# Kernel optimization log

Measured on AMD Instinct MI355X. Metric: run time of the kernel, lower is better.

## Reference

```python
import jax, jax.numpy as jnp
import numpy as np

N_EMBD = 512
HEAD_SIZE = 64
END_TOKEN = 32000  # == vocab_size


def setup_inputs() -> dict:
    key = jax.random.key(0)
    k1, k2, k3, k4, k5 = jax.random.split(key, 5)
    B, T = 16, 2048
    x = jax.random.normal(k1, (B, T, N_EMBD), dtype=jnp.float32)
    idx = jax.random.randint(k2, (B, T), 0, END_TOKEN)  # never hits END_TOKEN
    s = 1.0 / np.sqrt(N_EMBD)
    Wk = jax.random.normal(k3, (N_EMBD, HEAD_SIZE), dtype=jnp.float32) * s
    Wq = jax.random.normal(k4, (N_EMBD, HEAD_SIZE), dtype=jnp.float32) * s
    Wv = jax.random.normal(k5, (N_EMBD, HEAD_SIZE), dtype=jnp.float32) * s
    return {"x": x, "Wk": Wk, "Wq": Wq, "Wv": Wv, "idx": idx}


def reference(x, Wk, Wq, Wv, idx):
    B, T, C = x.shape
    k = x @ Wk  # [B,T,H]
    q = x @ Wq
    v = x @ Wv
    # end-token mask: zero out query rows at positions >= first end-token position
    is_end = idx == END_TOKEN                       # [B,T]
    has_end = jnp.any(is_end, axis=1)               # [B]
    first_end = jnp.argmax(is_end, axis=1)          # [B], 0 if none
    pos = jnp.arange(T)
    row_ok = jnp.where(has_end[:, None], pos[None, :] < first_end[:, None], True)  # [B,T]
    causal = jnp.tril(jnp.ones((T, T), dtype=bool))
    mask = causal[None, :, :] & row_ok[:, :, None]  # [B,T,T]
    # NOTE: original scales by C**-0.5 with C = n_embd, not head_size
    wei = jnp.einsum('bqh,bkh->bqk', q, k) * (C ** -0.5)
    wei = jnp.where(mask, wei, -jnp.inf)
    wei = jax.nn.softmax(wei, axis=-1)
    out = jnp.einsum('bqk,bkh->bqh', wei, v)  # [B,T,H]
    return out
```

## Files before the change

kernel.cpp:

```cpp
#include <hip/hip_runtime.h>
#include <hip/hip_bf16.h>


#define B_ 16
#define T_ 2048
#define C_ 512
#define LOG2E 1.4426950408889634f

typedef __attribute__((ext_vector_type(4))) float f32x4;
typedef __attribute__((ext_vector_type(8))) short bf16x8;

__device__ inline unsigned short f2bf(float f) {
    unsigned int u = __builtin_bit_cast(unsigned int, f);
    u += 0x7fff + ((u >> 16) & 1);
    return (unsigned short)(u >> 16);
}

__device__ inline f32x4 mfma16(bf16x8 a, bf16x8 b, f32x4 c) {
    return __builtin_amdgcn_mfma_f32_16x16x32_bf16(a, b, c, 0, 0, 0);
}

__global__ void prep_kernel(const float* __restrict__ Wk, const float* __restrict__ Wq,
                            const float* __restrict__ Wv, unsigned short* __restrict__ Wt,
                            int* __restrict__ fe) {
    if (blockIdx.x == 384) {
        if (threadIdx.x < B_) fe[threadIdx.x] = T_;
        return;
    }
    int id = blockIdx.x * 256 + threadIdx.x;
    int n = id >> 9, k = id & 511;
    int mtx = n >> 6, nl = n & 63;
    const float* W = (mtx == 0) ? Wk : ((mtx == 1) ? Wq : Wv);
    float v = W[k * 64 + nl];
    if (mtx == 1) v *= 0.04419417382415922f;
    Wt[n * 512 + k] = f2bf(v);
}

__global__ void scan_kernel(const int* __restrict__ idx, int* __restrict__ fe) {
    int i = blockIdx.x * 256 + threadIdx.x;
    if (idx[i] == 32000) atomicMin(&fe[i >> 11], i & 2047);
}

__global__ __launch_bounds__(256) void qkv_kernel(
        const float* __restrict__ x, const unsigned short* __restrict__ Wt,
        unsigned short* __restrict__ Qm, unsigned short* __restrict__ Km,
        unsigned short* __restrict__ Vt) {
    __shared__ __align__(16) char smem[32768];
    unsigned short* xs  = (unsigned short*)smem;
    unsigned short* wsh = (unsigned short*)(smem + 8192);
    unsigned short* co  = (unsigned short*)smem;
    unsigned short* vco = (unsigned short*)(smem + 17408);

    int tid = threadIdx.x, wave = tid >> 6, lane = tid & 63;
    int m16 = lane & 15, quad = lane >> 4;
    int row0 = blockIdx.x * 64;

    int xrow[2], xcol[2], wrow[6], wcol[6];
#pragma unroll
    for (int i = 0; i < 2; i++) { int u = tid + i * 256; xrow[i] = u >> 3; xcol[i] = (u & 7) * 8; }
#pragma unroll
    for (int i = 0; i < 6; i++) { int u = tid + i * 256; wrow[i] = u >> 3; wcol[i] = (u & 7) * 8; }

    f32x4 xa[2][2]; bf16x8 wr[6];
#pragma unroll
    for (int i = 0; i < 2; i++) {
        const f32x4* p = (const f32x4*)(x + (long)(row0 + xrow[i]) * C_ + xcol[i]);
        xa[i][0] = p[0]; xa[i][1] = p[1];
    }
#pragma unroll
    for (int i = 0; i < 6; i++) wr[i] = *(const bf16x8*)&Wt[wrow[i] * C_ + wcol[i]];

    f32x4 ka[4], qa[4], va[4];
#pragma unroll
    for (int i = 0; i < 4; i++) {
        ka[i] = (f32x4){0.f, 0.f, 0.f, 0.f};
        qa[i] = (f32x4){0.f, 0.f, 0.f, 0.f};
        va[i] = (f32x4){0.f, 0.f, 0.f, 0.f};
    }

    for (int kb = 0; kb < C_; kb += 64) {
        __syncthreads();
#pragma unroll
        for (int i = 0; i < 2; i++) {
            bf16x8 t;
#pragma unroll
            for (int j = 0; j < 4; j++) t[j] = (short)f2bf(xa[i][0][j]);
#pragma unroll
            for (int j = 0; j < 4; j++) t[4 + j] = (short)f2bf(xa[i][1][j]);
            *(bf16x8*)&xs[xrow[i] * 64 + (xcol[i] ^ ((xrow[i] & 7) * 8))] = t;
        }
#pragma unroll
        for (int i = 0; i < 6; i++)
            *(bf16x8*)&wsh[wrow[i] * 64 + (wcol[i] ^ ((wrow[i] & 7) * 8))] = wr[i];
        int kn = kb + 64;
        if (kn < C_) {
#pragma unroll
            for (int i = 0; i < 2; i++) {
                const f32x4* p = (const f32x4*)(x + (long)(row0 + xrow[i]) * C_ + kn + xcol[i]);
                xa[i][0] = p[0]; xa[i][1] = p[1];
            }
#pragma unroll
            for (int i = 0; i < 6; i++) wr[i] = *(const bf16x8*)&Wt[wrow[i] * C_ + kn + wcol[i]];
        }
        __syncthreads();
#pragma unroll
        for (int ks = 0; ks < 2; ks++) {
            int ko = ks * 32 + quad * 8;
            bf16x8 xf[4];
#pragma unroll
            for (int mt = 0; mt < 4; mt++) {
                int ar = mt * 16 + m16;
                xf[mt] = *(const bf16x8*)&xs[ar * 64 + (ko ^ ((ar & 7) * 8))];
            }
            int kr = wave * 16 + m16, qr = 64 + wave * 16 + m16, vr = 128 + wave * 16 + m16;
            bf16x8 wk = *(const bf16x8*)&wsh[kr * 64 + (ko ^ ((kr & 7) * 8))];
            bf16x8 wq = *(const bf16x8*)&wsh[qr * 64 + (ko ^ ((qr & 7) * 8))];
            bf16x8 wv = *(const bf16x8*)&wsh[vr * 64 + (ko ^ ((vr & 7) * 8))];
#pragma unroll
            for (int mt = 0; mt < 4; mt++) ka[mt] = mfma16(xf[mt], wk, ka[mt]);
#pragma unroll
            for (int mt = 0; mt < 4; mt++) qa[mt] = mfma16(xf[mt], wq, qa[mt]);
#pragma unroll
            for (int mt = 0; mt < 4; mt++) va[mt] = mfma16(wv, xf[mt], va[mt]);
        }
    }
    __syncthreads();

#pragma unroll
    for (int mt = 0; mt < 4; mt++) {
        int trow = mt * 16 + quad * 4;
#pragma unroll
        for (int r = 0; r < 4; r++) {
            co[(trow + r) * 136 + wave * 16 + m16]      = f2bf(ka[mt][r]);
            co[(trow + r) * 136 + 64 + wave * 16 + m16] = f2bf(qa[mt][r]);
            vco[wave * 1152 + (quad * 4 + r) * 72 + mt * 16 + m16] = f2bf(va[mt][r]);
        }
    }
    __syncthreads();
#pragma unroll
    for (int i = 0; i < 4; i++) {
        int u = tid + i * 256; int tok = u >> 4; int fg = u & 15;
        bf16x8 vv = *(const bf16x8*)&co[tok * 136 + fg * 8];
        unsigned short* dst = (fg < 8) ? Km : Qm;
        *(bf16x8*)&dst[(long)(row0 + tok) * 64 + (fg & 7) * 8] = vv;
    }
    int bb = row0 >> 11, tl = row0 & 2047;
#pragma unroll
    for (int i = 0; i < 2; i++) {
        int u = lane + i * 64; int hl = u >> 3; int tg = u & 7;
        bf16x8 vv = *(const bf16x8*)&vco[wave * 1152 + hl * 72 + tg * 8];
        *(bf16x8*)&Vt[((long)bb * 64 + wave * 16 + hl) * T_ + tl + tg * 8] = vv;
    }
}

__global__ __launch_bounds__(512, 4) void attn_kernel(
        const unsigned short* __restrict__ Qm, const unsigned short* __restrict__ Km,
        const unsigned short* __restrict__ Vt, const int* __restrict__ fe,
        float* __restrict__ out) {
    __shared__ __align__(16) unsigned short Klds[2][2][64 * 64];
    __shared__ __align__(16) unsigned short Vlds[2][2][64 * 64];
    __shared__ __align__(16) unsigned short Plds[8][16 * 64];

    int id = blockIdx.x;
    int j = id & 255, hi = id >> 8;
    int qt = hi ? 31 - (j >> 3) : (j >> 3);
    int b = (j & 7) | (hi << 3);

    int tid = threadIdx.x, wave = tid >> 6, lane = tid & 63;
    int g = wave >> 2, wg = wave & 3;
    int m16 = lane & 15, quad = lane >> 4;
    int row0 = qt * 64;
    long bT = (long)b * T_;

    int n = qt + 1;
    int n0 = (n + 1) >> 1;
    int n1 = n - n0;
    int ng = g ? n1 : n0;
    int kbase = g ? n0 : 0;
    int nloop = n0;

    int gtid = wg * 64 + lane;
    int srow[2], sk8[2], ssw[2];
#pragma unroll
    for (int c = 0; c < 2; c++) {
        int cc = gtid + c * 256;
        srow[c] = cc >> 3; sk8[c] = (cc & 7) * 8;
        ssw[c] = sk8[c] ^ ((srow[c] & 7) * 8);
    }

    const unsigned short* qp = Qm + (bT + row0 + wg * 16 + m16) * 64;
    bf16x8 qf0 = *(const bf16x8*)(qp + quad * 8);
    bf16x8 qf1 = *(const bf16x8*)(qp + 32 + quad * 8);

    f32x4 o[5];
#pragma unroll
    for (int h = 0; h < 5; h++) o[h] = (f32x4){0.f, 0.f, 0.f, 0.f};
    float mi[4];
#pragma unroll
    for (int r = 0; r < 4; r++) mi[r] = -INFINITY;
    int qloc = row0 + wg * 16 + quad * 4;

    bf16x8 onesb;
    {
        short ov = (m16 == 0) ? (short)0x3F80 : (short)0;
#pragma unroll
        for (int jj = 0; jj < 8; jj++) onesb[jj] = ov;
    }

    unsigned short (*Kg)[64 * 64] = Klds[g];
    unsigned short (*Vg)[64 * 64] = Vlds[g];

    bf16x8 kp[2], vp[2];
    if (ng > 0) {
        long c0 = (long)kbase * 64;
#pragma unroll
        for (int c = 0; c < 2; c++) {
            kp[c] = *(const bf16x8*)&Km[(bT + c0 + srow[c]) * 64 + sk8[c]];
            vp[c] = *(const bf16x8*)&Vt[((long)b * 64 + srow[c]) * T_ + c0 + sk8[c]];
        }
#pragma unroll
        for (int c = 0; c < 2; c++) {
            *(bf16x8*)&Kg[0][srow[c] * 64 + ssw[c]] = kp[c];
            *(bf16x8*)&Vg[0][srow[c] * 64 + ssw[c]] = vp[c];
        }
    }

    for (int it = 0; it < nloop; ++it) {
        int cur = it & 1;
        bool active = it < ng;
        int kt = kbase + it;
        bool pf = active && (it + 1 < ng);
        if (pf) {
            long cn = (long)(kt + 1) * 64;
#pragma unroll
            for (int c = 0; c < 2; c++) {
                kp[c] = *(const bf16x8*)&Km[(bT + cn + srow[c]) * 64 + sk8[c]];
                vp[c] = *(const bf16x8*)&Vt[((long)b * 64 + srow[c]) * T_ + cn + sk8[c]];
            }
        }
        __syncthreads();
        if (active) {
            const unsigned short* Kb = Kg[cur];
            const unsigned short* Vb = Vg[cur];

            f32x4 s[4];
#pragma unroll
            for (int ns = 0; ns < 4; ns++) {
                int krow = ns * 16 + m16;
                int swz = (krow & 7) * 8;
                bf16x8 kf0 = *(const bf16x8*)&Kb[krow * 64 + ((quad * 8) ^ swz)];
                bf16x8 kf1 = *(const bf16x8*)&Kb[krow * 64 + ((32 + quad * 8) ^ swz)];
                f32x4 z = (f32x4){0.f, 0.f, 0.f, 0.f};
                z = mfma16(qf0, kf0, z);
                z = mfma16(qf1, kf1, z);
                s[ns] = z;
            }

            bool diag = (kt == qt);
#pragma unroll
            for (int r = 0; r < 4; r++) {
                int qpos = qloc + r;
                if (diag) {
#pragma unroll
                    for (int ns = 0; ns < 4; ns++) {
                        int nn = kt * 64 + ns * 16 + m16;
                        if (nn > qpos) s[ns][r] = -INFINITY;
                    }
                }
                float mx = fmaxf(fmaxf(s[0][r], s[1][r]), fmaxf(s[2][r], s[3][r]));
                mx = fmaxf(mx, mi[r]);
#pragma unroll
                for (int off = 1; off < 16; off <<= 1)
                    mx = fmaxf(mx, __shfl_xor(mx, off));
                float alpha = exp2f((mi[r] - mx) * LOG2E);
                mi[r] = mx;
#pragma unroll
                for (int ns = 0; ns < 4; ns++)
                    s[ns][r] = exp2f((s[ns][r] - mx) * LOG2E);
#pragma unroll
                for (int h = 0; h < 5; h++) o[h][r] *= alpha;
            }

            unsigned short* pw = Plds[wave];
#pragma unroll
            for (int ns = 0; ns < 4; ns++)
#pragma unroll
                for (int r = 0; r < 4; r++) {
                    int mrow = quad * 4 + r;
                    int nn = ns * 16 + m16;
                    pw[mrow * 64 + (nn ^ ((mrow & 7) * 8))] = f2bf(s[ns][r]);
                }

            int aswz = (m16 & 7) * 8;
            bf16x8 pa0 = *(const bf16x8*)&pw[m16 * 64 + ((quad * 8) ^ aswz)];
            bf16x8 pa1 = *(const bf16x8*)&pw[m16 * 64 + ((32 + quad * 8) ^ aswz)];
#pragma unroll
            for (int hs = 0; hs < 4; hs++) {
                int vrow = hs * 16 + m16;
                int vswz = (vrow & 7) * 8;
                bf16x8 vb0 = *(const bf16x8*)&Vb[vrow * 64 + ((quad * 8) ^ vswz)];
                bf16x8 vb1 = *(const bf16x8*)&Vb[vrow * 64 + ((32 + quad * 8) ^ vswz)];
                o[hs] = mfma16(pa0, vb0, o[hs]);
                o[hs] = mfma16(pa1, vb1, o[hs]);
            }
            o[4] = mfma16(pa0, onesb, o[4]);
            o[4] = mfma16(pa1, onesb, o[4]);
        }
        if (pf) {
            int nxt = 1 - cur;
#pragma unroll
            for (int c = 0; c < 2; c++) {
                *(bf16x8*)&Kg[nxt][srow[c] * 64 + ssw[c]] = kp[c];
                *(bf16x8*)&Vg[nxt][srow[c] * 64 + ssw[c]] = vp[c];
            }
        }
    }

    __syncthreads();
    float* Po = (float*)&Klds[0][0][0];
    float* Pm = Po + 64 * 68;
    float* Pl = Pm + 64;
    if (g == 1) {
#pragma unroll
        for (int r = 0; r < 4; r++) {
            int row = wg * 16 + quad * 4 + r;
#pragma unroll
            for (int hs = 0; hs < 4; hs++)
                Po[row * 68 + hs * 16 + m16] = o[hs][r];
            if (m16 == 0) { Pm[row] = mi[r]; Pl[row] = o[4][r]; }
        }
    }
    __syncthreads();
    if (g == 0) {
        int feb = fe[b];
#pragma unroll
        for (int r = 0; r < 4; r++) {
            int row = wg * 16 + quad * 4 + r;
            int t = row0 + row;
            float m1v = Pm[row], l1v = Pl[row];
            float mm = fmaxf(mi[r], m1v);
            float a0 = exp2f((mi[r] - mm) * LOG2E);
            float a1 = exp2f((m1v - mm) * LOG2E);
            float l0 = __shfl(o[4][r], lane & 48);
            float inv = 1.0f / (l0 * a0 + l1v * a1);
            bool dead = (t >= feb);
#pragma unroll
            for (int hs = 0; hs < 4; hs++) {
                float val = dead ? __builtin_nanf("")
                                 : (o[hs][r] * a0 + Po[row * 68 + hs * 16 + m16] * a1) * inv;
                out[(bT + t) * 64 + hs * 16 + m16] = val;
            }
        }
    }
}

extern "C" void kernel_launch(void* const* d_in, const int* in_sizes, int n_in,
                              void* d_out, int out_size, void* d_ws, size_t ws_size,
                              hipStream_t stream) {
    const float* x  = (const float*)d_in[0];
    const float* Wk = (const float*)d_in[1];
    const float* Wq = (const float*)d_in[2];
    const float* Wv = (const float*)d_in[3];
    const int* idx  = (const int*)d_in[4];
    float* out = (float*)d_out;

    char* ws = (char*)d_ws;
    int* fe            = (int*)ws;
    unsigned short* Wt = (unsigned short*)(ws + 1024);
    unsigned short* Qm = (unsigned short*)(ws + 262144);
    unsigned short* Km = (unsigned short*)(ws + 262144 + 4194304);
    unsigned short* Vt = (unsigned short*)(ws + 262144 + 8388608);

    prep_kernel<<<385, 256, 0, stream>>>(Wk, Wq, Wv, Wt, fe);
    scan_kernel<<<128, 256, 0, stream>>>(idx, fe);
    qkv_kernel<<<512, 256, 0, stream>>>(x, Wt, Qm, Km, Vt);
    attn_kernel<<<512, 512, 0, stream>>>(Qm, Km, Vt, fe, out);
}
```

Baseline: 154.7 us.

## Fold log2e into Q scale, lazy softmax rescale, packed bf16 conversions

Folds log2(e) into the Q weight scale so the exp2 arguments no longer need a multiply. Skips the running-max update and accumulator rescale when every row's new max stays within 8 (log2 units) of the old one, which removes per-tile rescaling. Replaces the scalar float-to-bf16 rounding with the hardware v_cvt_pk_bf16_f32 instruction in both the QKV and attention kernels. It also moves barriers so global prefetch loads are issued after the barrier. The lazy rescale lets un-normalised values grow up to 2^8, which costs some accuracy headroom.

```diff
diff --git a/kernel.cpp b/kernel.cpp
--- a/kernel.cpp
+++ b/kernel.cpp
@@ -5,15 +5,21 @@
 #define B_ 16
 #define T_ 2048
 #define C_ 512
-#define LOG2E 1.4426950408889634f
 
 typedef __attribute__((ext_vector_type(4))) float f32x4;
 typedef __attribute__((ext_vector_type(8))) short bf16x8;
+typedef __attribute__((ext_vector_type(4))) unsigned int u32x4;
 
 __device__ inline unsigned short f2bf(float f) {
     unsigned int u = __builtin_bit_cast(unsigned int, f);
     u += 0x7fff + ((u >> 16) & 1);
     return (unsigned short)(u >> 16);
+}
+
+__device__ inline unsigned int cvt_pk_bf16(float lo, float hi) {
+    unsigned int r;
+    asm("v_cvt_pk_bf16_f32 %0, %1, %2" : "=v"(r) : "v"(lo), "v"(hi));
+    return r;
 }
 
 __device__ inline f32x4 mfma16(bf16x8 a, bf16x8 b, f32x4 c) {
@@ -32,7 +38,7 @@
     int mtx = n >> 6, nl = n & 63;
     const float* W = (mtx == 0) ? Wk : ((mtx == 1) ? Wq : Wv);
     float v = W[k * 64 + nl];
-    if (mtx == 1) v *= 0.04419417382415922f;
+    if (mtx == 1) v *= 0.0637587166f;
     Wt[n * 512 + k] = f2bf(v);
 }
 
@@ -82,16 +88,17 @@
         __syncthreads();
 #pragma unroll
         for (int i = 0; i < 2; i++) {
-            bf16x8 t;
-#pragma unroll
-            for (int j = 0; j < 4; j++) t[j] = (short)f2bf(xa[i][0][j]);
-#pragma unroll
-            for (int j = 0; j < 4; j++) t[4 + j] = (short)f2bf(xa[i][1][j]);
-            *(bf16x8*)&xs[xrow[i] * 64 + (xcol[i] ^ ((xrow[i] & 7) * 8))] = t;
+            u32x4 t;
+            t[0] = cvt_pk_bf16(xa[i][0][0], xa[i][0][1]);
+            t[1] = cvt_pk_bf16(xa[i][0][2], xa[i][0][3]);
+            t[2] = cvt_pk_bf16(xa[i][1][0], xa[i][1][1]);
+            t[3] = cvt_pk_bf16(xa[i][1][2], xa[i][1][3]);
+            *(u32x4*)&xs[xrow[i] * 64 + (xcol[i] ^ ((xrow[i] & 7) * 8))] = t;
         }
 #pragma unroll
         for (int i = 0; i < 6; i++)
             *(bf16x8*)&wsh[wrow[i] * 64 + (wcol[i] ^ ((wrow[i] & 7) * 8))] = wr[i];
+        __syncthreads();
         int kn = kb + 64;
         if (kn < C_) {
 #pragma unroll
@@ -102,7 +109,6 @@
 #pragma unroll
             for (int i = 0; i < 6; i++) wr[i] = *(const bf16x8*)&Wt[wrow[i] * C_ + kn + wcol[i]];
         }
-        __syncthreads();
 #pragma unroll
         for (int ks = 0; ks < 2; ks++) {
             int ko = ks * 32 + quad * 8;
@@ -230,6 +236,7 @@
         bool active = it < ng;
         int kt = kbase + it;
         bool pf = active && (it + 1 < ng);
+        __syncthreads();
         if (pf) {
             long cn = (long)(kt + 1) * 64;
 #pragma unroll
@@ -238,7 +245,6 @@
                 vp[c] = *(const bf16x8*)&Vt[((long)b * 64 + srow[c]) * T_ + cn + sk8[c]];
             }
         }
-        __syncthreads();
         if (active) {
             const unsigned short* Kb = Kg[cur];
             const unsigned short* Vb = Vg[cur];
@@ -257,6 +263,7 @@
             }
 
             bool diag = (kt == qt);
+            float pmax[4];
 #pragma unroll
             for (int r = 0; r < 4; r++) {
                 int qpos = qloc + r;
@@ -268,28 +275,45 @@
                     }
                 }
                 float mx = fmaxf(fmaxf(s[0][r], s[1][r]), fmaxf(s[2][r], s[3][r]));
-                mx = fmaxf(mx, mi[r]);
 #pragma unroll
                 for (int off = 1; off < 16; off <<= 1)
                     mx = fmaxf(mx, __shfl_xor(mx, off));
-                float alpha = exp2f((mi[r] - mx) * LOG2E);
-                mi[r] = mx;
-#pragma unroll
-                for (int ns = 0; ns < 4; ns++)
-                    s[ns][r] = exp2f((s[ns][r] - mx) * LOG2E);
-#pragma unroll
-                for (int h = 0; h < 5; h++) o[h][r] *= alpha;
+                pmax[r] = mx;
+            }
+            bool cnd = (pmax[0] <= mi[0] + 8.f) && (pmax[1] <= mi[1] + 8.f)
+                    && (pmax[2] <= mi[2] + 8.f) && (pmax[3] <= mi[3] + 8.f);
+            if (__all(cnd)) {
+#pragma unroll
+                for (int r = 0; r < 4; r++)
+#pragma unroll
+                    for (int ns = 0; ns < 4; ns++)
+                        s[ns][r] = exp2f(s[ns][r] - mi[r]);
+            } else {
+#pragma unroll
+                for (int r = 0; r < 4; r++) {
+                    float mx = fmaxf(pmax[r], mi[r]);
+                    float alpha = exp2f(mi[r] - mx);
+                    mi[r] = mx;
+#pragma unroll
+                    for (int ns = 0; ns < 4; ns++)
+                        s[ns][r] = exp2f(s[ns][r] - mx);
+#pragma unroll
+                    for (int h = 0; h < 5; h++) o[h][r] *= alpha;
+                }
             }
 
             unsigned short* pw = Plds[wave];
 #pragma unroll
-            for (int ns = 0; ns < 4; ns++)
-#pragma unroll
-                for (int r = 0; r < 4; r++) {
-                    int mrow = quad * 4 + r;
-                    int nn = ns * 16 + m16;
-                    pw[mrow * 64 + (nn ^ ((mrow & 7) * 8))] = f2bf(s[ns][r]);
-                }
+            for (int r = 0; r < 4; r++) {
+                int mrow = quad * 4 + r;
+                int swzr = (mrow & 7) * 8;
+                unsigned int p01 = cvt_pk_bf16(s[0][r], s[1][r]);
+                unsigned int p23 = cvt_pk_bf16(s[2][r], s[3][r]);
+                pw[mrow * 64 + ((m16) ^ swzr)]      = (unsigned short)(p01 & 0xffffu);
+                pw[mrow * 64 + ((16 + m16) ^ swzr)] = (unsigned short)(p01 >> 16);
+                pw[mrow * 64 + ((32 + m16) ^ swzr)] = (unsigned short)(p23 & 0xffffu);
+                pw[mrow * 64 + ((48 + m16) ^ swzr)] = (unsigned short)(p23 >> 16);
+            }
 
             int aswz = (m16 & 7) * 8;
             bf16x8 pa0 = *(const bf16x8*)&pw[m16 * 64 + ((quad * 8) ^ aswz)];
@@ -339,8 +363,8 @@
             int t = row0 + row;
             float m1v = Pm[row], l1v = Pl[row];
             float mm = fmaxf(mi[r], m1v);
-            float a0 = exp2f((mi[r] - mm) * LOG2E);
-            float a1 = exp2f((m1v - mm) * LOG2E);
+            float a0 = exp2f(mi[r] - mm);
+            float a1 = exp2f(m1v - mm);
             float l0 = __shfl(o[4][r], lane & 48);
             float inv = 1.0f / (l0 * a0 + l1v * a1);
             bool dead = (t >= feb);
```

Measured after the change: 197.9 us. +27.9%, slower.
